# Kernel tuning notes

Measured on AMD Instinct MI355X. Metric: run time of the kernel, lower is better.

The kernel has to match this reference:

```python
import jax, jax.numpy as jnp
import numpy as np

NUM_STATES = 16
INPUT_DIM = 1024
QUANTUM_DIM = 1024
LN_EPS = 1e-5


def setup_inputs() -> dict:
    key = jax.random.key(0)
    ks = jax.random.split(key, 7)
    # stacked per-state Linear weights: [S, input_dim, quantum_dim]
    W = jax.random.normal(ks[0], (NUM_STATES, INPUT_DIM, QUANTUM_DIM), jnp.float32) * (1.0 / np.sqrt(INPUT_DIM))
    b = jax.random.normal(ks[1], (NUM_STATES, QUANTUM_DIM), jnp.float32) * 0.01
    amplitude_weights = jax.random.normal(ks[2], (NUM_STATES, QUANTUM_DIM), jnp.float32)
    phase_weights = jax.random.normal(ks[3], (NUM_STATES, QUANTUM_DIM), jnp.float32)
    ln_gamma = jnp.ones((QUANTUM_DIM,), jnp.float32)
    ln_beta = jnp.zeros((QUANTUM_DIM,), jnp.float32)
    language_features = jax.random.normal(ks[4], (4096, INPUT_DIM), jnp.float32)
    return {
        "language_features": language_features,
        "W": W,
        "b": b,
        "amplitude_weights": amplitude_weights,
        "phase_weights": phase_weights,
        "ln_gamma": ln_gamma,
        "ln_beta": ln_beta,
    }


def reference(language_features, W, b, amplitude_weights, phase_weights, ln_gamma, ln_beta):
    # Per-state linear projections as one batched GEMM: [B, S, Q]
    states = jnp.einsum("bi,siq->bsq", language_features, W) + b[None, :, :]
    # amplitudes = softmax over states (dim=0 in torch)
    amplitudes = jax.nn.softmax(amplitude_weights, axis=0)  # [S, Q]
    # real(amplitude * exp(i*phase) * state) = amplitude * cos(phase) * state
    mix = amplitudes * jnp.cos(phase_weights)  # [S, Q]
    sup = states * mix[None, :, :]  # [B, S, Q]
    # LayerNorm over last dim
    mean = jnp.mean(sup, axis=-1, keepdims=True)
    var = jnp.var(sup, axis=-1, keepdims=True)
    out = (sup - mean) * jax.lax.rsqrt(var + LN_EPS) * ln_gamma + ln_beta
    return out
```

## Files before the change

### kernel.cpp

```cpp
#include <hip/hip_runtime.h>

typedef __attribute__((ext_vector_type(8))) short short8;
typedef __attribute__((ext_vector_type(4))) float f32x4;
typedef __attribute__((ext_vector_type(4))) unsigned short u16x4;

#define GLOAD16(g, l)                                                          \
  __builtin_amdgcn_global_load_lds(                                            \
      (const __attribute__((address_space(1))) unsigned int*)(g),              \
      (__attribute__((address_space(3))) unsigned int*)(l), 16, 0, 0)

__device__ __forceinline__ unsigned short f2bf(float f) {
  unsigned int u = __float_as_uint(f);
  u += 0x7FFFu + ((u >> 16) & 1u);
  return (unsigned short)(u >> 16);
}
__device__ __forceinline__ float bf2f(unsigned short h) {
  return __uint_as_float(((unsigned int)h) << 16);
}

__global__ void mix_kernel(const float* __restrict__ amp,
                           const float* __restrict__ phase,
                           const float* __restrict__ bias,
                           float* __restrict__ mix, float* __restrict__ bmix) {
  int q = blockIdx.x * blockDim.x + threadIdx.x;
  float a[16];
  float mx = -1e30f;
  for (int s = 0; s < 16; ++s) {
    a[s] = amp[s * 1024 + q];
    mx = fmaxf(mx, a[s]);
  }
  float sum = 0.f;
  for (int s = 0; s < 16; ++s) {
    a[s] = __expf(a[s] - mx);
    sum += a[s];
  }
  float inv = 1.f / sum;
  for (int s = 0; s < 16; ++s) {
    float m = a[s] * inv * cosf(phase[s * 1024 + q]);
    mix[s * 1024 + q] = m;
    bmix[s * 1024 + q] = bias[s * 1024 + q] * m;
  }
}

__global__ void cast_x_kernel(const float* __restrict__ x,
                              unsigned short* __restrict__ xb) {
  int i = (blockIdx.x * blockDim.x + threadIdx.x) * 4;
  float4 v = *(const float4*)(x + i);
  union { unsigned short h[4]; uint2 u; } o;
  o.h[0] = f2bf(v.x); o.h[1] = f2bf(v.y); o.h[2] = f2bf(v.z); o.h[3] = f2bf(v.w);
  *(uint2*)(xb + i) = o.u;
}

__global__ __launch_bounds__(256) void transpose_w_kernel(
    const float* __restrict__ W, const float* __restrict__ mix,
    unsigned short* __restrict__ Wt) {
  __shared__ unsigned short tile[64][68];
  const int s = blockIdx.z;
  const int q0 = blockIdx.x * 64, i0 = blockIdx.y * 64;
  const int t = threadIdx.x;
  const float* Ws = W + (size_t)s * 1048576;
  unsigned short* Wts = Wt + (size_t)s * 1048576;
  const int rq = (t & 15) * 4;
  const int ri = t >> 4;
  const float4 mv = *(const float4*)(mix + s * 1024 + q0 + rq);
  #pragma unroll
  for (int p = 0; p < 4; ++p) {
    const int i = p * 16 + ri;
    float4 v = *(const float4*)(Ws + (size_t)(i0 + i) * 1024 + q0 + rq);
    union { unsigned short h[4]; uint2 u; } pk;
    pk.h[0] = f2bf(v.x * mv.x);
    pk.h[1] = f2bf(v.y * mv.y);
    pk.h[2] = f2bf(v.z * mv.z);
    pk.h[3] = f2bf(v.w * mv.w);
    *(uint2*)&tile[i][rq] = pk.u;
  }
  __syncthreads();
  const int wq = t >> 2;
  const int wi = (t & 3) * 16;
  union { unsigned short h[8]; short8 v8; } u0, u1;
  #pragma unroll
  for (int e = 0; e < 8; ++e) {
    u0.h[e] = tile[wi + e][wq];
    u1.h[e] = tile[wi + 8 + e][wq];
  }
  unsigned short* dst = Wts + (size_t)(q0 + wq) * 1024 + i0 + wi;
  *(short8*)dst = u0.v8;
  *(short8*)(dst + 8) = u1.v8;
}

template <bool BF16SUP>
__global__ __launch_bounds__(256) void gemm_kernel(
    const unsigned short* __restrict__ xb, const unsigned short* __restrict__ wt,
    const float* __restrict__ bmix,
    float* __restrict__ outf, unsigned short* __restrict__ sup) {
  __shared__ __align__(16) unsigned short Abuf[3][128 * 32];
  __shared__ __align__(16) unsigned short Bbuf[3][128 * 32];

  const int tid = threadIdx.x;
  const int lane = tid & 63;
  const int wv = tid >> 6;
  const int wm = wv >> 1, wn = wv & 1;
  const int m0 = blockIdx.y * 128;
  const int n0 = blockIdx.x * 128;

  const int c0 = tid, c1 = tid + 256;
  const int r0 = c0 >> 2, k80 = (c0 & 3) * 8;
  const int r1 = c1 >> 2, k81 = (c1 & 3) * 8;
  const unsigned short* ga0 = xb + (size_t)(m0 + r0) * 1024 + k80;
  const unsigned short* ga1 = xb + (size_t)(m0 + r1) * 1024 + k81;
  const unsigned short* gb0 = wt + (size_t)(n0 + r0) * 1024 + k80;
  const unsigned short* gb1 = wt + (size_t)(n0 + r1) * 1024 + k81;

#define STAGE(kt, b) do {                                                      \
    const int _ko = (kt) * 32;                                                 \
    GLOAD16(ga0 + _ko, &Abuf[b][c0 * 8]);                                      \
    GLOAD16(ga1 + _ko, &Abuf[b][c1 * 8]);                                      \
    GLOAD16(gb0 + _ko, &Bbuf[b][c0 * 8]);                                      \
    GLOAD16(gb1 + _ko, &Bbuf[b][c1 * 8]);                                      \
  } while (0)

  f32x4 acc[4][4];
  #pragma unroll
  for (int i = 0; i < 4; ++i)
    #pragma unroll
    for (int j = 0; j < 4; ++j) acc[i][j] = (f32x4){0.f, 0.f, 0.f, 0.f};

  STAGE(0, 0);
  STAGE(1, 1);
  asm volatile("s_waitcnt vmcnt(4)" ::: "memory");
  __builtin_amdgcn_s_barrier();

  const int lr = lane & 15;
  const int lk = (lane >> 4) * 8;
  int cur = 0;
  for (int kt = 0; kt < 32; ++kt) {
    if (kt < 30) {
      int nb = cur + 2; if (nb >= 3) nb -= 3;
      STAGE(kt + 2, nb);
    }
    short8 af[4], bfr[4];
    #pragma unroll
    for (int mi = 0; mi < 4; ++mi)
      af[mi] = *(const short8*)&Abuf[cur][(wm * 64 + mi * 16 + lr) * 32 + lk];
    #pragma unroll
    for (int ni = 0; ni < 4; ++ni)
      bfr[ni] = *(const short8*)&Bbuf[cur][(wn * 64 + ni * 16 + lr) * 32 + lk];
    asm volatile("s_waitcnt lgkmcnt(0)" ::: "memory");
    if (kt < 30) {
      asm volatile("s_waitcnt vmcnt(4)" ::: "memory");
    } else if (kt == 30) {
      asm volatile("s_waitcnt vmcnt(0)" ::: "memory");
    }
    __builtin_amdgcn_sched_barrier(0);
    __builtin_amdgcn_s_barrier();
    #pragma unroll
    for (int mi = 0; mi < 4; ++mi)
      #pragma unroll
      for (int ni = 0; ni < 4; ++ni)
        acc[mi][ni] = __builtin_amdgcn_mfma_f32_16x16x32_bf16(
            af[mi], bfr[ni], acc[mi][ni], 0, 0, 0);
    cur += 1; if (cur >= 3) cur = 0;
  }
#undef STAGE

  #pragma unroll
  for (int ni = 0; ni < 4; ++ni) {
    const int n = n0 + wn * 64 + ni * 16 + lr;
    const float bv = bmix[n];
    #pragma unroll
    for (int mi = 0; mi < 4; ++mi) {
      const int m = m0 + wm * 64 + mi * 16 + (lane >> 4) * 4;
      #pragma unroll
      for (int r = 0; r < 4; ++r) {
        float v = acc[mi][ni][r] + bv;
        if (BF16SUP)
          sup[(size_t)(m + r) * 16384 + n] = f2bf(v);
        else
          outf[(size_t)(m + r) * 16384 + n] = v;
      }
    }
  }
}

__global__ __launch_bounds__(256) void ln_bf16_kernel(
    const unsigned short* __restrict__ sup, float* __restrict__ out,
    const float* __restrict__ gamma, const float* __restrict__ beta) {
  __shared__ float red[8];
  const int t = threadIdx.x;
  const size_t base = (size_t)blockIdx.x * 1024;
  u16x4 raw = *(const u16x4*)(sup + base + t * 4);
  float v[4];
  #pragma unroll
  for (int j = 0; j < 4; ++j) v[j] = bf2f(raw[j]);
  float s = v[0] + v[1] + v[2] + v[3];
  float ss = v[0] * v[0] + v[1] * v[1] + v[2] * v[2] + v[3] * v[3];
  #pragma unroll
  for (int m = 32; m >= 1; m >>= 1) {
    s += __shfl_xor(s, m);
    ss += __shfl_xor(ss, m);
  }
  const int wv = t >> 6;
  if ((t & 63) == 0) { red[wv * 2] = s; red[wv * 2 + 1] = ss; }
  __syncthreads();
  const float S = red[0] + red[2] + red[4] + red[6];
  const float SS = red[1] + red[3] + red[5] + red[7];
  const float mean = S * (1.0f / 1024.0f);
  const float var = SS * (1.0f / 1024.0f) - mean * mean;
  const float rstd = rsqrtf(var + 1e-5f);
  const float4 g = *(const float4*)(gamma + t * 4);
  const float4 b = *(const float4*)(beta + t * 4);
  float4 o;
  o.x = (v[0] - mean) * rstd * g.x + b.x;
  o.y = (v[1] - mean) * rstd * g.y + b.y;
  o.z = (v[2] - mean) * rstd * g.z + b.z;
  o.w = (v[3] - mean) * rstd * g.w + b.w;
  *(float4*)(out + base + t * 4) = o;
}

__global__ __launch_bounds__(256) void ln_kernel(float* __restrict__ out,
                                                 const float* __restrict__ gamma,
                                                 const float* __restrict__ beta) {
  __shared__ float red[8];
  const int t = threadIdx.x;
  const size_t base = (size_t)blockIdx.x * 1024;
  float4 v = *(const float4*)(out + base + t * 4);
  float s = v.x + v.y + v.z + v.w;
  float ss = v.x * v.x + v.y * v.y + v.z * v.z + v.w * v.w;
  #pragma unroll
  for (int m = 32; m >= 1; m >>= 1) {
    s += __shfl_xor(s, m);
    ss += __shfl_xor(ss, m);
  }
  const int wv = t >> 6;
  if ((t & 63) == 0) { red[wv * 2] = s; red[wv * 2 + 1] = ss; }
  __syncthreads();
  const float S = red[0] + red[2] + red[4] + red[6];
  const float SS = red[1] + red[3] + red[5] + red[7];
  const float mean = S * (1.0f / 1024.0f);
  const float var = SS * (1.0f / 1024.0f) - mean * mean;
  const float rstd = rsqrtf(var + 1e-5f);
  const float4 g = *(const float4*)(gamma + t * 4);
  const float4 b = *(const float4*)(beta + t * 4);
  float4 o;
  o.x = (v.x - mean) * rstd * g.x + b.x;
  o.y = (v.y - mean) * rstd * g.y + b.y;
  o.z = (v.z - mean) * rstd * g.z + b.z;
  o.w = (v.w - mean) * rstd * g.w + b.w;
  *(float4*)(out + base + t * 4) = o;
}

extern "C" void kernel_launch(void* const* d_in, const int* in_sizes, int n_in,
                              void* d_out, int out_size, void* d_ws, size_t ws_size,
                              hipStream_t stream) {
  (void)in_sizes; (void)n_in; (void)out_size;
  const float* x     = (const float*)d_in[0];
  const float* W     = (const float*)d_in[1];
  const float* bias  = (const float*)d_in[2];
  const float* amp   = (const float*)d_in[3];
  const float* phase = (const float*)d_in[4];
  const float* gamma = (const float*)d_in[5];
  const float* beta  = (const float*)d_in[6];
  float* out = (float*)d_out;

  const bool big = ws_size >= (size_t)134217728ULL;

  unsigned short *Wt, *xbuf, *supb = nullptr;
  float *mixp, *bmixp;
  if (big) {
    char* ob = (char*)d_out;
    Wt    = (unsigned short*)ob;
    xbuf  = (unsigned short*)(ob + 33554432);
    mixp  = (float*)(ob + 41943040);
    bmixp = mixp + 16384;
    supb  = (unsigned short*)d_ws;
  } else {
    char* ws = (char*)d_ws;
    Wt    = (unsigned short*)ws;
    xbuf  = (unsigned short*)(ws + 33554432);
    mixp  = (float*)(ws + 33554432 + 8388608);
    bmixp = mixp + 16384;
  }

  hipLaunchKernelGGL(mix_kernel, dim3(4), dim3(256), 0, stream, amp, phase, bias, mixp, bmixp);
  hipLaunchKernelGGL(cast_x_kernel, dim3(4096), dim3(256), 0, stream, x, xbuf);
  hipLaunchKernelGGL(transpose_w_kernel, dim3(16, 16, 16), dim3(256), 0, stream, W, mixp, Wt);
  if (big) {
    hipLaunchKernelGGL((gemm_kernel<true>), dim3(128, 32), dim3(256), 0, stream,
                       xbuf, Wt, bmixp, out, supb);
    hipLaunchKernelGGL(ln_bf16_kernel, dim3(65536), dim3(256), 0, stream,
                       supb, out, gamma, beta);
  } else {
    hipLaunchKernelGGL((gemm_kernel<false>), dim3(128, 32), dim3(256), 0, stream,
                       xbuf, Wt, bmixp, out, nullptr);
    hipLaunchKernelGGL(ln_kernel, dim3(65536), dim3(256), 0, stream, out, gamma, beta);
  }
}
```

Baseline: 299.4 us.

## Widen GEMM tile to 128x256 with 8 waves and process two rows per LN block

Result: faster. 278.0 us (-7.1%).

```diff
diff --git a/kernel.cpp b/kernel.cpp
--- a/kernel.cpp
+++ b/kernel.cpp
@@ -89,34 +89,33 @@
 }
 
 template <bool BF16SUP>
-__global__ __launch_bounds__(256) void gemm_kernel(
+__global__ __launch_bounds__(512) void gemm_kernel(
     const unsigned short* __restrict__ xb, const unsigned short* __restrict__ wt,
     const float* __restrict__ bmix,
     float* __restrict__ outf, unsigned short* __restrict__ sup) {
   __shared__ __align__(16) unsigned short Abuf[3][128 * 32];
-  __shared__ __align__(16) unsigned short Bbuf[3][128 * 32];
+  __shared__ __align__(16) unsigned short Bbuf[3][256 * 32];
 
   const int tid = threadIdx.x;
   const int lane = tid & 63;
   const int wv = tid >> 6;
-  const int wm = wv >> 1, wn = wv & 1;
+  const int wm = wv >> 2, wn = wv & 3;
   const int m0 = blockIdx.y * 128;
-  const int n0 = blockIdx.x * 128;
-
-  const int c0 = tid, c1 = tid + 256;
-  const int r0 = c0 >> 2, k80 = (c0 & 3) * 8;
-  const int r1 = c1 >> 2, k81 = (c1 & 3) * 8;
-  const unsigned short* ga0 = xb + (size_t)(m0 + r0) * 1024 + k80;
-  const unsigned short* ga1 = xb + (size_t)(m0 + r1) * 1024 + k81;
-  const unsigned short* gb0 = wt + (size_t)(n0 + r0) * 1024 + k80;
-  const unsigned short* gb1 = wt + (size_t)(n0 + r1) * 1024 + k81;
+  const int n0 = blockIdx.x * 256;
+
+  const int rA = tid >> 2, kA = (tid & 3) * 8;
+  const unsigned short* gA = xb + (size_t)(m0 + rA) * 1024 + kA;
+  const int cB0 = tid, cB1 = tid + 512;
+  const int rB0 = cB0 >> 2, kB0 = (cB0 & 3) * 8;
+  const int rB1 = cB1 >> 2, kB1 = (cB1 & 3) * 8;
+  const unsigned short* gB0 = wt + (size_t)(n0 + rB0) * 1024 + kB0;
+  const unsigned short* gB1 = wt + (size_t)(n0 + rB1) * 1024 + kB1;
 
 #define STAGE(kt, b) do {                                                      \
     const int _ko = (kt) * 32;                                                 \
-    GLOAD16(ga0 + _ko, &Abuf[b][c0 * 8]);                                      \
-    GLOAD16(ga1 + _ko, &Abuf[b][c1 * 8]);                                      \
-    GLOAD16(gb0 + _ko, &Bbuf[b][c0 * 8]);                                      \
-    GLOAD16(gb1 + _ko, &Bbuf[b][c1 * 8]);                                      \
+    GLOAD16(gA + _ko, &Abuf[b][tid * 8]);                                      \
+    GLOAD16(gB0 + _ko, &Bbuf[b][cB0 * 8]);                                     \
+    GLOAD16(gB1 + _ko, &Bbuf[b][cB1 * 8]);                                     \
   } while (0)
 
   f32x4 acc[4][4];
@@ -127,7 +126,7 @@
 
   STAGE(0, 0);
   STAGE(1, 1);
-  asm volatile("s_waitcnt vmcnt(4)" ::: "memory");
+  asm volatile("s_waitcnt vmcnt(3)" ::: "memory");
   __builtin_amdgcn_s_barrier();
 
   const int lr = lane & 15;
@@ -147,7 +146,7 @@
       bfr[ni] = *(const short8*)&Bbuf[cur][(wn * 64 + ni * 16 + lr) * 32 + lk];
     asm volatile("s_waitcnt lgkmcnt(0)" ::: "memory");
     if (kt < 30) {
-      asm volatile("s_waitcnt vmcnt(4)" ::: "memory");
+      asm volatile("s_waitcnt vmcnt(3)" ::: "memory");
     } else if (kt == 30) {
       asm volatile("s_waitcnt vmcnt(0)" ::: "memory");
     }
@@ -187,34 +186,47 @@
     const float* __restrict__ gamma, const float* __restrict__ beta) {
   __shared__ float red[8];
   const int t = threadIdx.x;
-  const size_t base = (size_t)blockIdx.x * 1024;
-  u16x4 raw = *(const u16x4*)(sup + base + t * 4);
-  float v[4];
-  #pragma unroll
-  for (int j = 0; j < 4; ++j) v[j] = bf2f(raw[j]);
-  float s = v[0] + v[1] + v[2] + v[3];
-  float ss = v[0] * v[0] + v[1] * v[1] + v[2] * v[2] + v[3] * v[3];
+  const int half = t >> 7;
+  const int j = t & 127;
+  const size_t base = ((size_t)blockIdx.x * 2 + half) * 1024;
+  union { short8 v8; unsigned short h[8]; } raw;
+  raw.v8 = *(const short8*)(sup + base + j * 8);
+  float v[8];
+  float s = 0.f, ss = 0.f;
+  #pragma unroll
+  for (int e = 0; e < 8; ++e) {
+    v[e] = bf2f(raw.h[e]);
+    s += v[e];
+    ss += v[e] * v[e];
+  }
   #pragma unroll
   for (int m = 32; m >= 1; m >>= 1) {
     s += __shfl_xor(s, m);
     ss += __shfl_xor(ss, m);
   }
-  const int wv = t >> 6;
-  if ((t & 63) == 0) { red[wv * 2] = s; red[wv * 2 + 1] = ss; }
+  const int wvi = t >> 6;
+  if ((t & 63) == 0) { red[wvi * 2] = s; red[wvi * 2 + 1] = ss; }
   __syncthreads();
-  const float S = red[0] + red[2] + red[4] + red[6];
-  const float SS = red[1] + red[3] + red[5] + red[7];
+  const float S = red[half * 4] + red[half * 4 + 2];
+  const float SS = red[half * 4 + 1] + red[half * 4 + 3];
   const float mean = S * (1.0f / 1024.0f);
   const float var = SS * (1.0f / 1024.0f) - mean * mean;
   const float rstd = rsqrtf(var + 1e-5f);
-  const float4 g = *(const float4*)(gamma + t * 4);
-  const float4 b = *(const float4*)(beta + t * 4);
-  float4 o;
-  o.x = (v[0] - mean) * rstd * g.x + b.x;
-  o.y = (v[1] - mean) * rstd * g.y + b.y;
-  o.z = (v[2] - mean) * rstd * g.z + b.z;
-  o.w = (v[3] - mean) * rstd * g.w + b.w;
-  *(float4*)(out + base + t * 4) = o;
+  const float4 g0 = *(const float4*)(gamma + j * 8);
+  const float4 g1 = *(const float4*)(gamma + j * 8 + 4);
+  const float4 b0 = *(const float4*)(beta + j * 8);
+  const float4 b1 = *(const float4*)(beta + j * 8 + 4);
+  float4 o0, o1;
+  o0.x = (v[0] - mean) * rstd * g0.x + b0.x;
+  o0.y = (v[1] - mean) * rstd * g0.y + b0.y;
+  o0.z = (v[2] - mean) * rstd * g0.z + b0.z;
+  o0.w = (v[3] - mean) * rstd * g0.w + b0.w;
+  o1.x = (v[4] - mean) * rstd * g1.x + b1.x;
+  o1.y = (v[5] - mean) * rstd * g1.y + b1.y;
+  o1.z = (v[6] - mean) * rstd * g1.z + b1.z;
+  o1.w = (v[7] - mean) * rstd * g1.w + b1.w;
+  *(float4*)(out + base + j * 8) = o0;
+  *(float4*)(out + base + j * 8 + 4) = o1;
 }
 
 __global__ __launch_bounds__(256) void ln_kernel(float* __restrict__ out,
@@ -285,12 +297,12 @@
   hipLaunchKernelGGL(cast_x_kernel, dim3(4096), dim3(256), 0, stream, x, xbuf);
   hipLaunchKernelGGL(transpose_w_kernel, dim3(16, 16, 16), dim3(256), 0, stream, W, mixp, Wt);
   if (big) {
-    hipLaunchKernelGGL((gemm_kernel<true>), dim3(128, 32), dim3(256), 0, stream,
+    hipLaunchKernelGGL((gemm_kernel<true>), dim3(64, 32), dim3(512), 0, stream,
                        xbuf, Wt, bmixp, out, supb);
-    hipLaunchKernelGGL(ln_bf16_kernel, dim3(65536), dim3(256), 0, stream,
+    hipLaunchKernelGGL(ln_bf16_kernel, dim3(32768), dim3(256), 0, stream,
                        supb, out, gamma, beta);
   } else {
-    hipLaunchKernelGGL((gemm_kernel<false>), dim3(128, 32), dim3(256), 0, stream,
+    hipLaunchKernelGGL((gemm_kernel<false>), dim3(64, 32), dim3(512), 0, stream,
                        xbuf, Wt, bmixp, out, nullptr);
     hipLaunchKernelGGL(ln_kernel, dim3(65536), dim3(256), 0, stream, out, gamma, beta);
   }
```
